# Kernel optimization log

Measured on AMD Instinct MI355X. Metric: run time of the kernel, lower is better.

## Reference

```python
import jax, jax.numpy as jnp
import numpy as np

TEMPERATURE = 0.5
W_WITHIN = 1.0
W_CROSS = 0.5
MARGIN = 0.1


def setup_inputs() -> dict:
    key = jax.random.key(0)
    k1, k2 = jax.random.split(key)
    features = jax.random.normal(k1, (8192, 256), dtype=jnp.float32)
    gene_labels = jax.random.randint(k2, (8192,), 0, 200, dtype=jnp.int64 if jax.config.jax_enable_x64 else jnp.int32)
    return {"features": features, "gene_labels": gene_labels}


def reference(features, gene_labels):
    B = features.shape[0]
    # L2-normalize rows, full pairwise cosine similarity / temperature
    fn = features / jnp.linalg.norm(features, axis=1, keepdims=True)
    sim = (fn @ fn.T) / TEMPERATURE  # [B, B]

    same = gene_labels[:, None] == gene_labels[None, :]  # [B, B]
    eye = jnp.eye(B, dtype=bool)
    same_off = same & ~eye            # same-gene, off-diagonal (gene_similarity)
    neg = ~same                       # different-gene pairs (cross_gene_mask)
    has_neg = neg.any(axis=1)

    # Per-anchor logsumexp over negatives (sim of anchor i to all different-gene samples)
    neg_sim = jnp.where(neg, sim, -jnp.inf)
    lse_neg = jax.scipy.special.logsumexp(neg_sim, axis=1)
    lse_neg = jnp.where(has_neg, lse_neg, 0.0)  # rows with no negatives are masked out below

    # Within-gene loss: for each unordered same-gene pair (i<j) with gene != -1 and
    # anchor i having >=1 negative: CE([sim_ij, neg_sims_i], label=0)
    #   = -sim_ij + logaddexp(sim_ij, lse_neg_i) = softplus(lse_neg_i - sim_ij)
    upper = jnp.triu(jnp.ones((B, B), dtype=bool), k=1)
    valid_gene = (gene_labels != -1)[:, None]
    pair_mask = same_off & upper & valid_gene & has_neg[:, None]
    within_gene_loss = jnp.where(pair_mask, jax.nn.softplus(lse_neg[:, None] - sim), 0.0).sum()

    # Cross-gene loss: mean over all ordered different-gene pairs of relu(sim - margin)
    cross_cnt = neg.sum()
    cross_sum = jnp.where(neg, jax.nn.relu(sim - MARGIN), 0.0).sum()
    cross_gene_loss = jnp.where(cross_cnt > 0, cross_sum / jnp.maximum(cross_cnt, 1).astype(sim.dtype), 0.0)

    total_loss = W_WITHIN * within_gene_loss + W_CROSS * cross_gene_loss
    num_within_gene_pairs = same_off.sum().astype(sim.dtype)
    num_cross_gene_pairs = cross_cnt
    return total_loss, within_gene_loss, cross_gene_loss, num_within_gene_pairs, num_cross_gene_pairs
```

## Files before the change

### kernel.cpp

```cpp
#include <hip/hip_runtime.h>
#include <math.h>

#define B_N   8192
#define D_K   256
#define NGENE 200
#define MAXN  512

typedef short  bf16x8 __attribute__((ext_vector_type(8)));
typedef float  f32x4  __attribute__((ext_vector_type(4)));

#define OFF_FNBF    0u
#define OFF_LPART   4194304u
#define OFF_HIST    4718592u
#define OFF_OFFS    4719616u
#define OFF_SORTED  4720640u
#define OFF_CROSSP  4753408u
#define OFF_WITHINP 4755456u
#define OFF_CCORR   4756480u

__device__ __forceinline__ unsigned short f2bf(float f) {
    unsigned int u = __float_as_uint(f);
    unsigned int r = u + 0x7fffu + ((u >> 16) & 1u);
    return (unsigned short)(r >> 16);
}
__device__ __forceinline__ float bf2f_lo(unsigned int u) { return __uint_as_float(u << 16); }
__device__ __forceinline__ float bf2f_hi(unsigned int u) { return __uint_as_float(u & 0xffff0000u); }

__global__ __launch_bounds__(256) void k_norm(const float* __restrict__ feat,
                                              const int* __restrict__ lab,
                                              unsigned short* __restrict__ fnbf,
                                              int* __restrict__ hist) {
    int wave = threadIdx.x >> 6, lane = threadIdx.x & 63;
    int row  = blockIdx.x * 4 + wave;
    const float4* src = reinterpret_cast<const float4*>(feat + (size_t)row * D_K);
    float4 v = src[lane];
    float ss = v.x * v.x + v.y * v.y + v.z * v.z + v.w * v.w;
#pragma unroll
    for (int m = 1; m < 64; m <<= 1) ss += __shfl_xor(ss, m);
    float rn = 1.0f / sqrtf(ss);
    ushort4 o;
    o.x = f2bf(v.x * rn); o.y = f2bf(v.y * rn);
    o.z = f2bf(v.z * rn); o.w = f2bf(v.w * rn);
    reinterpret_cast<ushort4*>(fnbf + (size_t)row * D_K)[lane] = o;
    if (lane == 0) {
        int lb = lab[row];
        if (lb >= 0 && lb < NGENE) atomicAdd(&hist[lb], 1);
    }
}

__global__ __launch_bounds__(256) void k_scatter(const int* __restrict__ lab,
                                                 const int* __restrict__ hist,
                                                 int* __restrict__ offs,
                                                 int* __restrict__ sorted) {
    int g = blockIdx.x, t = threadIdx.x;
    __shared__ int sc[256];

    int hv = (t < NGENE) ? hist[t] : 0;
    sc[t] = hv;
    __syncthreads();
#pragma unroll
    for (int d = 1; d < 256; d <<= 1) {
        int x = (t >= d) ? sc[t - d] : 0;
        __syncthreads();
        sc[t] += x;
        __syncthreads();
    }
    int start = (g == 0) ? 0 : sc[g - 1];
    if (t == 0) offs[g] = start;
    __syncthreads();

    int r0 = t * 32, cnt = 0;
    for (int r = r0; r < r0 + 32; ++r) cnt += (lab[r] == g) ? 1 : 0;
    sc[t] = cnt;
    __syncthreads();
#pragma unroll
    for (int d = 1; d < 256; d <<= 1) {
        int x = (t >= d) ? sc[t - d] : 0;
        __syncthreads();
        sc[t] += x;
        __syncthreads();
    }
    int w = start + sc[t] - cnt;
    for (int r = r0; r < r0 + 32; ++r)
        if (lab[r] == g) sorted[w++] = r;
}

#define GLOAD8(arr, vo) do {                                                                   \
    asm volatile("global_load_dwordx4 %0, %1, %2 offset:0"   : "=v"(arr[0]) : "v"(vo), "s"(fb)); \
    asm volatile("global_load_dwordx4 %0, %1, %2 offset:64"  : "=v"(arr[1]) : "v"(vo), "s"(fb)); \
    asm volatile("global_load_dwordx4 %0, %1, %2 offset:128" : "=v"(arr[2]) : "v"(vo), "s"(fb)); \
    asm volatile("global_load_dwordx4 %0, %1, %2 offset:192" : "=v"(arr[3]) : "v"(vo), "s"(fb)); \
    asm volatile("global_load_dwordx4 %0, %1, %2 offset:256" : "=v"(arr[4]) : "v"(vo), "s"(fb)); \
    asm volatile("global_load_dwordx4 %0, %1, %2 offset:320" : "=v"(arr[5]) : "v"(vo), "s"(fb)); \
    asm volatile("global_load_dwordx4 %0, %1, %2 offset:384" : "=v"(arr[6]) : "v"(vo), "s"(fb)); \
    asm volatile("global_load_dwordx4 %0, %1, %2 offset:448" : "=v"(arr[7]) : "v"(vo), "s"(fb)); \
} while (0)

#define GL_LDS16(gp, lp)                                                          \
    __builtin_amdgcn_global_load_lds(                                             \
        (const __attribute__((address_space(1))) unsigned int*)(gp),              \
        (__attribute__((address_space(3))) unsigned int*)(lp), 16, 0, 0)

#define Z4 ((f32x4){0.f, 0.f, 0.f, 0.f})
#define MFMA(A, B, C) __builtin_amdgcn_mfma_f32_16x16x32_bf16(A, B, C, 0, 0, 0)

#define EPI(AC, LS, CS) do {                                    \
    _Pragma("unroll")                                           \
    for (int r = 0; r < 4; ++r) {                               \
        float av = AC[r];                                       \
        LS[r] += __expf(2.0f * av);                             \
        CS += fmaxf(av - 0.05f, 0.f);                           \
    }                                                           \
} while (0)

#define WAIT_VM(n) do { asm volatile("s_waitcnt vmcnt(" #n ")" ::: "memory"); \
                        __builtin_amdgcn_sched_barrier(0); } while (0)

#define WAIT_LGKM0 do { asm volatile("s_waitcnt lgkmcnt(0)" ::: "memory"); \
                        __builtin_amdgcn_sched_barrier(0); } while (0)

#define STAGE_W(BOFF, T) do {                                                      \
    const char* gt = gw + (unsigned)(T) * 8192u;                                   \
    _Pragma("unroll")                                                              \
    for (int q = 0; q < 8; ++q)                                                    \
        GL_LDS16(gt + sv[q], smem_c + wbase + (BOFF) + q * 1024u);                 \
} while (0)

__global__ __launch_bounds__(256, 2) void k_pairwise(const unsigned short* __restrict__ fnbf,
                                                     float* __restrict__ l_part,
                                                     float* __restrict__ cross_part) {
    __shared__ __align__(16) char smem_c[65536];
    __shared__ float shc[4];

    int tid = threadIdx.x;
    int wave = tid >> 6, lane = tid & 63;
    int g16 = lane >> 4, l16 = lane & 15;
    int l7 = l16 & 7;
    int rg = blockIdx.x, cwin = blockIdx.y;
    int r0 = rg * 256 + wave * 64;
    const unsigned short* fb = fnbf;
    unsigned wbase = (unsigned)wave * 16384u;

    bf16x8 a0[8], a1[8], a2[8], a3[8];
    unsigned voa = (unsigned)(r0 + l16) * 512u + (unsigned)g16 * 16u;
    GLOAD8(a0, voa); voa += 8192u;
    GLOAD8(a1, voa); voa += 8192u;
    GLOAD8(a2, voa); voa += 8192u;
    GLOAD8(a3, voa);

    const char* gw = (const char*)fnbf + (size_t)cwin * 262144u;
    unsigned sv[8];
#pragma unroll
    for (int q = 0; q < 8; ++q) {
        int f = q * 64 + lane;
        int col = f >> 5;
        sv[q] = (unsigned)(col * 512 + (((lane & 31) ^ (col & 7)) << 4));
    }

    STAGE_W(0u, 0);
    STAGE_W(8192u, 1);
    WAIT_VM(16);

    float lsum[4][4] = {};
    float cs0 = 0.f, cs1 = 0.f, cs2 = 0.f, cs3 = 0.f;
    int vb = l16 * 512;

#pragma unroll 1
    for (int st = 0; st < 32; ++st) {
        if (st < 31) { WAIT_VM(8); }
        else         { WAIT_VM(0); }

        const char* base = smem_c + wbase + (unsigned)((st & 1) << 13);
        f32x4 acc0 = Z4, acc1 = Z4, acc2 = Z4, acc3 = Z4;
#pragma unroll
        for (int ks = 0; ks < 8; ++ks) {
            const char* p = base + (unsigned)(vb + ((((ks << 2) | g16) ^ l7) << 4));
            bf16x8 bv = *(const bf16x8*)p;
            acc0 = MFMA(a0[ks], bv, acc0);
            acc1 = MFMA(a1[ks], bv, acc1);
            acc2 = MFMA(a2[ks], bv, acc2);
            acc3 = MFMA(a3[ks], bv, acc3);
        }
        EPI(acc0, lsum[0], cs0); EPI(acc1, lsum[1], cs1);
        EPI(acc2, lsum[2], cs2); EPI(acc3, lsum[3], cs3);

        if (st < 30) {
            WAIT_LGKM0;
            STAGE_W((unsigned)((st & 1) << 13), st + 2);
        }
    }

#pragma unroll
    for (int t = 0; t < 4; ++t)
#pragma unroll
        for (int r = 0; r < 4; ++r) {
            float v = lsum[t][r];
            v += __shfl_xor(v, 1); v += __shfl_xor(v, 2);
            v += __shfl_xor(v, 4); v += __shfl_xor(v, 8);
            if (l16 == 0)
                l_part[(size_t)cwin * B_N + r0 + t * 16 + g16 * 4 + r] = v;
        }

    float c = (cs0 + cs1) + (cs2 + cs3);
#pragma unroll
    for (int m = 1; m < 64; m <<= 1) c += __shfl_xor(c, m);
    if (lane == 0) shc[wave] = c;
    __syncthreads();
    if (tid == 0)
        cross_part[cwin * 32 + rg] = shc[0] + shc[1] + shc[2] + shc[3];
}

__device__ __forceinline__ float dot_g(const uint4* __restrict__ fu, int i, int j) {
    const uint4* pa = fu + (size_t)i * 32;
    const uint4* pb = fu + (size_t)j * 32;
    float d = 0.f;
#pragma unroll
    for (int k = 0; k < 32; ++k) {
        uint4 ua = pa[k], ub = pb[k];
        d = fmaf(bf2f_lo(ua.x), bf2f_lo(ub.x), d);
        d = fmaf(bf2f_hi(ua.x), bf2f_hi(ub.x), d);
        d = fmaf(bf2f_lo(ua.y), bf2f_lo(ub.y), d);
        d = fmaf(bf2f_hi(ua.y), bf2f_hi(ub.y), d);
        d = fmaf(bf2f_lo(ua.z), bf2f_lo(ub.z), d);
        d = fmaf(bf2f_hi(ua.z), bf2f_hi(ub.z), d);
        d = fmaf(bf2f_lo(ua.w), bf2f_lo(ub.w), d);
        d = fmaf(bf2f_hi(ua.w), bf2f_hi(ub.w), d);
    }
    return d;
}

__global__ __launch_bounds__(256) void k_within(const unsigned short* __restrict__ fnbf,
                                                const int* __restrict__ hist,
                                                const int* __restrict__ offs,
                                                const int* __restrict__ sorted,
                                                const float* __restrict__ l_part,
                                                float* __restrict__ within_part,
                                                float* __restrict__ cross_corr) {
    int g = blockIdx.x;
    int n = hist[g], start = offs[g];
    int t = threadIdx.x;
    int wave = t >> 6, lane = t & 63;
    int g16 = lane >> 4, l16 = lane & 15;

    __shared__ float sim[128 * 130];
    __shared__ int   rid[MAXN];
    __shared__ float slse[MAXN];
    __shared__ float red[256];

    for (int idx = t; idx < n; idx += 256) rid[idx] = sorted[start + idx];
    __syncthreads();

    float ccor = 0.f, wsum = 0.f;

    if (n <= 128) {
        int NT = (n + 15) >> 4;
        const bf16x8* fv = reinterpret_cast<const bf16x8*>(fnbf);
        for (int tile = wave; tile < NT * NT; tile += 4) {
            int ti = tile / NT, tj = tile - ti * NT;
            int ia = ti * 16 + l16;
            int ib = tj * 16 + l16;
            int ra = rid[ia < n ? ia : (n - 1)];
            int rb = rid[ib < n ? ib : (n - 1)];
            f32x4 acc = Z4;
#pragma unroll
            for (int ks = 0; ks < 8; ++ks) {
                bf16x8 av = fv[(size_t)ra * 32 + ks * 4 + g16];
                bf16x8 bv = fv[(size_t)rb * 32 + ks * 4 + g16];
                acc = MFMA(av, bv, acc);
            }
            int si = ti * 16 + g16 * 4;
            int sj = tj * 16 + l16;
#pragma unroll
            for (int r = 0; r < 4; ++r)
                sim[(si + r) * 130 + sj] = acc[r];
        }
        __syncthreads();

        for (int i = t; i < n; i += 256) {
            float raw = 0.f;
#pragma unroll
            for (int k = 0; k < 16; ++k) raw += l_part[(size_t)k * B_N + rid[i]];
            const float* srow = &sim[i * 130];
            float esum = 0.f;
            for (int j = 0; j < n; ++j) {
                float s = 2.0f * srow[j];
                esum += __expf(s);
                ccor += fmaxf(s - 0.1f, 0.f);
            }
            slse[i] = __logf(raw - esum);
        }
        __syncthreads();

        int nn = n * n;
        for (int p = t; p < nn; p += 256) {
            int i = p / n, j = p - i * n;
            if (j <= i) continue;
            float s = 2.0f * sim[i * 130 + j];
            int ai = (rid[i] < rid[j]) ? i : j;
            float x = slse[ai] - s;
            wsum += fmaxf(x, 0.f) + log1pf(__expf(-fabsf(x)));
        }
    } else {
        const uint4* fu = reinterpret_cast<const uint4*>(fnbf);
        for (int i = t; i < n; i += 256) {
            float raw = 0.f;
#pragma unroll
            for (int k = 0; k < 16; ++k) raw += l_part[(size_t)k * B_N + rid[i]];
            float esum = 0.f;
            for (int j = 0; j < n; ++j) {
                float s = 2.0f * dot_g(fu, rid[i], rid[j]);
                esum += __expf(s);
                ccor += fmaxf(s - 0.1f, 0.f);
            }
            slse[i] = __logf(raw - esum);
        }
        __syncthreads();
        int nn = n * n;
        for (int p = t; p < nn; p += 256) {
            int i = p / n, j = p - i * n;
            if (j <= i) continue;
            float s = 2.0f * dot_g(fu, rid[i], rid[j]);
            int ai = (rid[i] < rid[j]) ? i : j;
            float x = slse[ai] - s;
            wsum += fmaxf(x, 0.f) + log1pf(__expf(-fabsf(x)));
        }
    }

    red[t] = wsum;
    __syncthreads();
#pragma unroll
    for (int d2 = 128; d2 > 0; d2 >>= 1) {
        if (t < d2) red[t] += red[t + d2];
        __syncthreads();
    }
    if (t == 0) within_part[g] = red[0];
    __syncthreads();
    red[t] = ccor;
    __syncthreads();
#pragma unroll
    for (int d2 = 128; d2 > 0; d2 >>= 1) {
        if (t < d2) red[t] += red[t + d2];
        __syncthreads();
    }
    if (t == 0) cross_corr[g] = red[0];
}

__global__ __launch_bounds__(256) void k_finalize(const float* __restrict__ cross_part,
                                                  const float* __restrict__ within_part,
                                                  const float* __restrict__ cross_corr,
                                                  const int* __restrict__ hist,
                                                  float* __restrict__ out) {
    __shared__ float shc[256];
    __shared__ float shw[256];
    __shared__ float shk[256];
    __shared__ long long shs[256];
    int t = threadIdx.x;
    float cs = 0.f;
    for (int i = t; i < 512; i += 256) cs += cross_part[i];
    float wv = 0.f, cc = 0.f;
    long long s2 = 0;
    if (t < NGENE) {
        wv = within_part[t];
        cc = cross_corr[t];
        long long h = hist[t];
        s2 = h * h;
    }
    shc[t] = cs; shw[t] = wv; shk[t] = cc; shs[t] = s2;
    __syncthreads();
#pragma unroll
    for (int d = 128; d > 0; d >>= 1) {
        if (t < d) {
            shc[t] += shc[t + d]; shw[t] += shw[t + d];
            shk[t] += shk[t + d]; shs[t] += shs[t + d];
        }
        __syncthreads();
    }
    if (t == 0) {
        long long S  = shs[0];
        long long nw = S - (long long)B_N;
        long long nc = (long long)B_N * (long long)B_N - S;
        float cross_total = 2.0f * shc[0] - shk[0];
        float cross_loss = (nc > 0) ? (cross_total / (float)(nc > 1 ? nc : 1)) : 0.f;
        float within     = shw[0];
        out[0] = within + 0.5f * cross_loss;
        out[1] = within;
        out[2] = cross_loss;
        out[3] = (float)nw;
        out[4] = (float)nc;
    }
}

extern "C" void kernel_launch(void* const* d_in, const int* in_sizes, int n_in,
                              void* d_out, int out_size, void* d_ws, size_t ws_size,
                              hipStream_t stream) {
    const float* feat = (const float*)d_in[0];
    const int*   lab  = (const int*)d_in[1];
    float* out = (float*)d_out;
    char* ws = (char*)d_ws;

    unsigned short* fnbf = (unsigned short*)(ws + OFF_FNBF);
    float* l_part        = (float*)(ws + OFF_LPART);
    int*   hist          = (int*)(ws + OFF_HIST);
    int*   offs          = (int*)(ws + OFF_OFFS);
    int*   sorted        = (int*)(ws + OFF_SORTED);
    float* cross_part    = (float*)(ws + OFF_CROSSP);
    float* within_part   = (float*)(ws + OFF_WITHINP);
    float* cross_corr    = (float*)(ws + OFF_CCORR);

    hipMemsetAsync(hist, 0, NGENE * sizeof(int), stream);
    k_norm<<<B_N / 4, 256, 0, stream>>>(feat, lab, fnbf, hist);
    k_scatter<<<NGENE, 256, 0, stream>>>(lab, hist, offs, sorted);
    k_pairwise<<<dim3(32, 16), 256, 0, stream>>>(fnbf, l_part, cross_part);
    k_within<<<NGENE, 256, 0, stream>>>(fnbf, hist, offs, sorted, l_part, within_part, cross_corr);
    k_finalize<<<1, 256, 0, stream>>>(cross_part, within_part, cross_corr, hist, out);
}
```

Measured before the change: 99.23 us.

## Merge prep kernels and fold finalize into last within-gene block

```diff
diff --git a/kernel.cpp b/kernel.cpp
--- a/kernel.cpp
+++ b/kernel.cpp
@@ -17,6 +17,7 @@
 #define OFF_CROSSP  4753408u
 #define OFF_WITHINP 4755456u
 #define OFF_CCORR   4756480u
+#define OFF_DONE    4757504u
 
 __device__ __forceinline__ unsigned short f2bf(float f) {
     unsigned int u = __float_as_uint(f);
@@ -26,37 +27,49 @@
 __device__ __forceinline__ float bf2f_lo(unsigned int u) { return __uint_as_float(u << 16); }
 __device__ __forceinline__ float bf2f_hi(unsigned int u) { return __uint_as_float(u & 0xffff0000u); }
 
-__global__ __launch_bounds__(256) void k_norm(const float* __restrict__ feat,
+__global__ __launch_bounds__(256) void k_prep(const float* __restrict__ feat,
                                               const int* __restrict__ lab,
                                               unsigned short* __restrict__ fnbf,
-                                              int* __restrict__ hist) {
-    int wave = threadIdx.x >> 6, lane = threadIdx.x & 63;
-    int row  = blockIdx.x * 4 + wave;
-    const float4* src = reinterpret_cast<const float4*>(feat + (size_t)row * D_K);
-    float4 v = src[lane];
-    float ss = v.x * v.x + v.y * v.y + v.z * v.z + v.w * v.w;
-#pragma unroll
-    for (int m = 1; m < 64; m <<= 1) ss += __shfl_xor(ss, m);
-    float rn = 1.0f / sqrtf(ss);
-    ushort4 o;
-    o.x = f2bf(v.x * rn); o.y = f2bf(v.y * rn);
-    o.z = f2bf(v.z * rn); o.w = f2bf(v.w * rn);
-    reinterpret_cast<ushort4*>(fnbf + (size_t)row * D_K)[lane] = o;
-    if (lane == 0) {
-        int lb = lab[row];
-        if (lb >= 0 && lb < NGENE) atomicAdd(&hist[lb], 1);
-    }
-}
-
-__global__ __launch_bounds__(256) void k_scatter(const int* __restrict__ lab,
-                                                 const int* __restrict__ hist,
-                                                 int* __restrict__ offs,
-                                                 int* __restrict__ sorted) {
-    int g = blockIdx.x, t = threadIdx.x;
+                                              int* __restrict__ hist,
+                                              int* __restrict__ offs,
+                                              int* __restrict__ sorted,
+                                              int* __restrict__ done) {
+    int b = blockIdx.x;
+    if (b < 2048) {
+        int wave = threadIdx.x >> 6, lane = threadIdx.x & 63;
+        int row  = b * 4 + wave;
+        const float4* src = reinterpret_cast<const float4*>(feat + (size_t)row * D_K);
+        float4 v = src[lane];
+        float ss = v.x * v.x + v.y * v.y + v.z * v.z + v.w * v.w;
+#pragma unroll
+        for (int m = 1; m < 64; m <<= 1) ss += __shfl_xor(ss, m);
+        float rn = 1.0f / sqrtf(ss);
+        ushort4 o;
+        o.x = f2bf(v.x * rn); o.y = f2bf(v.y * rn);
+        o.z = f2bf(v.z * rn); o.w = f2bf(v.w * rn);
+        reinterpret_cast<ushort4*>(fnbf + (size_t)row * D_K)[lane] = o;
+        return;
+    }
+    int g = b - 2048, t = threadIdx.x;
     __shared__ int sc[256];
-
-    int hv = (t < NGENE) ? hist[t] : 0;
-    sc[t] = hv;
+    if (g == 0 && t == 0) *done = 0;
+
+    int r0 = t * 32, lt = 0, eq = 0;
+    for (int r = r0; r < r0 + 32; ++r) {
+        int lb = lab[r];
+        lt += (lb >= 0 && lb < g) ? 1 : 0;
+        eq += (lb == g) ? 1 : 0;
+    }
+    sc[t] = lt;
+    __syncthreads();
+#pragma unroll
+    for (int d = 128; d > 0; d >>= 1) {
+        if (t < d) sc[t] += sc[t + d];
+        __syncthreads();
+    }
+    int start = sc[0];
+    __syncthreads();
+    sc[t] = eq;
     __syncthreads();
 #pragma unroll
     for (int d = 1; d < 256; d <<= 1) {
@@ -65,24 +78,11 @@
         sc[t] += x;
         __syncthreads();
     }
-    int start = (g == 0) ? 0 : sc[g - 1];
-    if (t == 0) offs[g] = start;
-    __syncthreads();
-
-    int r0 = t * 32, cnt = 0;
-    for (int r = r0; r < r0 + 32; ++r) cnt += (lab[r] == g) ? 1 : 0;
-    sc[t] = cnt;
-    __syncthreads();
-#pragma unroll
-    for (int d = 1; d < 256; d <<= 1) {
-        int x = (t >= d) ? sc[t - d] : 0;
-        __syncthreads();
-        sc[t] += x;
-        __syncthreads();
-    }
-    int w = start + sc[t] - cnt;
+    int w = start + sc[t] - eq;
     for (int r = r0; r < r0 + 32; ++r)
         if (lab[r] == g) sorted[w++] = r;
+    if (t == 0)   offs[g] = start;
+    if (t == 255) hist[g] = sc[255];
 }
 
 #define GLOAD8(arr, vo) do {                                                                   \
@@ -234,8 +234,11 @@
                                                 const int* __restrict__ offs,
                                                 const int* __restrict__ sorted,
                                                 const float* __restrict__ l_part,
+                                                const float* __restrict__ cross_part,
                                                 float* __restrict__ within_part,
-                                                float* __restrict__ cross_corr) {
+                                                float* __restrict__ cross_corr,
+                                                int* __restrict__ done,
+                                                float* __restrict__ out) {
     int g = blockIdx.x;
     int n = hist[g], start = offs[g];
     int t = threadIdx.x;
@@ -246,6 +249,7 @@
     __shared__ int   rid[MAXN];
     __shared__ float slse[MAXN];
     __shared__ float red[256];
+    __shared__ int   is_last;
 
     for (int idx = t; idx < n; idx += 256) rid[idx] = sorted[start + idx];
     __syncthreads();
@@ -343,18 +347,17 @@
         __syncthreads();
     }
     if (t == 0) cross_corr[g] = red[0];
-}
-
-__global__ __launch_bounds__(256) void k_finalize(const float* __restrict__ cross_part,
-                                                  const float* __restrict__ within_part,
-                                                  const float* __restrict__ cross_corr,
-                                                  const int* __restrict__ hist,
-                                                  float* __restrict__ out) {
-    __shared__ float shc[256];
-    __shared__ float shw[256];
-    __shared__ float shk[256];
-    __shared__ long long shs[256];
-    int t = threadIdx.x;
+
+    __syncthreads();
+    if (t == 0) {
+        __threadfence();
+        int prev = atomicAdd(done, 1);
+        is_last = (prev == NGENE - 1) ? 1 : 0;
+    }
+    __syncthreads();
+    if (!is_last) return;
+    __threadfence();
+
     float cs = 0.f;
     for (int i = t; i < 512; i += 256) cs += cross_part[i];
     float wv = 0.f, cc = 0.f;
@@ -365,6 +368,10 @@
         long long h = hist[t];
         s2 = h * h;
     }
+    float* shc = sim;
+    float* shw = sim + 256;
+    float* shk = sim + 512;
+    long long* shs = reinterpret_cast<long long*>(sim + 768);
     shc[t] = cs; shw[t] = wv; shk[t] = cc; shs[t] = s2;
     __syncthreads();
 #pragma unroll
@@ -406,11 +413,10 @@
     float* cross_part    = (float*)(ws + OFF_CROSSP);
     float* within_part   = (float*)(ws + OFF_WITHINP);
     float* cross_corr    = (float*)(ws + OFF_CCORR);
-
-    hipMemsetAsync(hist, 0, NGENE * sizeof(int), stream);
-    k_norm<<<B_N / 4, 256, 0, stream>>>(feat, lab, fnbf, hist);
-    k_scatter<<<NGENE, 256, 0, stream>>>(lab, hist, offs, sorted);
+    int*   done          = (int*)(ws + OFF_DONE);
+
+    k_prep<<<2048 + NGENE, 256, 0, stream>>>(feat, lab, fnbf, hist, offs, sorted, done);
     k_pairwise<<<dim3(32, 16), 256, 0, stream>>>(fnbf, l_part, cross_part);
-    k_within<<<NGENE, 256, 0, stream>>>(fnbf, hist, offs, sorted, l_part, within_part, cross_corr);
-    k_finalize<<<1, 256, 0, stream>>>(cross_part, within_part, cross_corr, hist, out);
-}
+    k_within<<<NGENE, 256, 0, stream>>>(fnbf, hist, offs, sorted, l_part, cross_part,
+                                        within_part, cross_corr, done, out);
+}
```

Result: faster. 85.11 us, median of 3 (-14.2%).
